# Kernel optimization log

Hardware: AMD Instinct MI355X
Metric: run time of the kernel (lower is better)

## Reference

```python
import jax, jax.numpy as jnp
import numpy as np

B, D, C, H, L = 32768, 64, 64, 1024, 6
EPS = 1e-5
NIN = (D - D // 2) + C  # unchanged half + cond = 96
SPLIT = D // 2          # 32


def setup_inputs() -> dict:
    key = jax.random.key(0)
    ks = jax.random.split(key, 12)
    s = 0.05
    return {
        "z": jax.random.normal(ks[0], (B, D), jnp.float32),
        "cond": jax.random.normal(ks[1], (B, C), jnp.float32),
        "W1": jax.random.normal(ks[2], (L, NIN, H), jnp.float32) * s,
        "b1": jax.random.normal(ks[3], (L, H), jnp.float32) * s,
        "W2": jax.random.normal(ks[4], (L, H, H), jnp.float32) * s,
        "b2": jax.random.normal(ks[5], (L, H), jnp.float32) * s,
        "Ws": jax.random.normal(ks[6], (L, H, SPLIT), jnp.float32) * s,
        "bs": jax.random.normal(ks[7], (L, SPLIT), jnp.float32) * s,
        "Wt": jax.random.normal(ks[8], (L, H, SPLIT), jnp.float32) * s,
        "bt": jax.random.normal(ks[9], (L, SPLIT), jnp.float32) * s,
        "bn_w": 1.0 + 0.1 * jax.random.normal(ks[10], (L, D), jnp.float32),
        "bn_b": 0.1 * jax.random.normal(ks[11], (L, D), jnp.float32),
    }


def reference(z, cond, W1, b1, W2, b2, Ws, bs, Wt, bt, bn_w, bn_b):
    x = z
    log_det = jnp.zeros((z.shape[0],), z.dtype)
    for i in range(L):
        # 'even' mask keeps even indices on even layers, odd indices otherwise
        if i % 2 == 0:
            keep, chg = np.arange(0, D, 2), np.arange(1, D, 2)
        else:
            keep, chg = np.arange(1, D, 2), np.arange(0, D, 2)
        # 2-layer MLP on [x_keep, cond]
        h = jax.nn.relu(jnp.concatenate([x[:, keep], cond], axis=1) @ W1[i] + b1[i])
        h = jax.nn.relu(h @ W2[i] + b2[i])
        log_s = jnp.tanh(h @ Ws[i] + bs[i])          # (B, SPLIT)
        t = h @ Wt[i] + bt[i]                         # (B, SPLIT)
        x2t = x[:, chg] * jnp.exp(log_s) + t
        x = jnp.zeros_like(x).at[:, keep].set(x[:, keep]).at[:, chg].set(x2t)
        log_det = log_det + log_s.sum(axis=1)
        # BatchNorm1d, training mode: batch mean / biased variance, eps=1e-5
        mean = x.mean(axis=0)
        var = x.var(axis=0)
        x = (x - mean) * jax.lax.rsqrt(var + EPS) * bn_w[i] + bn_b[i]
        log_det = log_det + jnp.log(jnp.abs(bn_w[i])).sum()
    return x, log_det
```

## Files before the change

kernel.cpp:

```cpp
#include <hip/hip_runtime.h>
#include <math.h>

#define BB 32768
#define DD 64
#define CC 64
#define HH 1024
#define LL 6
#define SPLIT 32
#define NIN 96
#define EPSV 1e-5f

typedef short short8 __attribute__((ext_vector_type(8)));
typedef float f32x4 __attribute__((ext_vector_type(4)));
typedef unsigned short u16;

__device__ __forceinline__ u16 f2bf(float f) {
    union { float f; unsigned int u; } c; c.f = f;
    unsigned int u = c.u + 0x7FFFu + ((c.u >> 16) & 1u);
    return (u16)(u >> 16);
}

__device__ __forceinline__ void gl_lds16(const u16* g, u16* l) {
    __builtin_amdgcn_global_load_lds(
        (const __attribute__((address_space(1))) unsigned int*)g,
        (__attribute__((address_space(3))) unsigned int*)l, 16, 0, 0);
}

#define DSR(dst, addr, off) \
    asm volatile("ds_read_b128 %0, %1 offset:" #off : "=&v"(dst) : "v"(addr))

__global__ void transpose_cvt_kernel(const float* __restrict__ src, u16* __restrict__ dst,
                                     int R, int C, int Rpad,
                                     long long sstride, long long dstride)
{
    __shared__ float tile[32][33];
    const float* s = src + (size_t)blockIdx.z * sstride;
    u16* d = dst + (size_t)blockIdx.z * dstride;
    int r0 = blockIdx.x * 32, c0 = blockIdx.y * 32;
    int tc = threadIdx.x & 31, tr = threadIdx.x >> 5;
#pragma unroll
    for (int i = 0; i < 4; ++i) {
        int r = r0 + tr + i * 8;
        tile[tr + i * 8][tc] = (r < R) ? s[(size_t)r * C + c0 + tc] : 0.f;
    }
    __syncthreads();
#pragma unroll
    for (int i = 0; i < 4; ++i) {
        int cc = tr + i * 8;
        d[(size_t)(c0 + cc) * Rpad + r0 + tc] = f2bf(tile[tc][cc]);
    }
}

__global__ __launch_bounds__(256)
void init_ain_cond_kernel(const float* __restrict__ cond, u16* __restrict__ Ain)
{
    int t = blockIdx.x * 256 + threadIdx.x;
    int c = t % 96, r = t / 96;
    Ain[(size_t)r * 128 + 32 + c] = (c < CC) ? f2bf(cond[(size_t)r * CC + c]) : (u16)0;
}

__global__ __launch_bounds__(256)
void build_keep_kernel(const float* __restrict__ x, u16* __restrict__ Ain, int keep_off)
{
    int t = blockIdx.x * 256 + threadIdx.x;
    int c = t & 31, r = t >> 5;
    Ain[(size_t)r * 128 + c] = f2bf(x[(size_t)r * DD + 2 * c + keep_off]);
}

__global__ __launch_bounds__(512, 2)
void gemm_tiled(const u16* __restrict__ A,
                const u16* __restrict__ Bt,
                const float* __restrict__ bias,
                u16* __restrict__ Cc,
                int K)
{
    __shared__ u16 sA[2][32 * 512];
    __shared__ u16 sB[2][32 * 512];

    const int t = threadIdx.x;
    const int w = t >> 6, lane = t & 63;
    const int lane16 = lane & 15, quad = lane >> 4;
    const int wm = w >> 2, wn = w & 3;

    int id = blockIdx.x;
    int nby = gridDim.x >> 2;
    int xcd = id & 7, slot = id >> 3;
    int bx = slot & 3, byq = slot >> 2;
    int by = xcd * (nby >> 3) + byq;
    const int bm = by * 256, bn = bx * 256;

    const int ntile = K >> 6;

    auto stage_half = [&](int kt, int op, int s, int buf) {
        int k0 = kt * 64 + s * 32 + quad * 8;
#pragma unroll
        for (int r = 0; r < 2; ++r) {
            int i = r * 8 + w;
            int e = s * 16 + i;
            if (op == 0) {
                const u16* g = A + (size_t)(bm + i * 16 + lane16) * K + k0;
                gl_lds16(g, &sA[buf][e * 512]);
            } else {
                const u16* g = Bt + (size_t)(bn + i * 16 + lane16) * K + k0;
                gl_lds16(g, &sB[buf][e * 512]);
            }
        }
    };

    f32x4 acc[8][4];
#pragma unroll
    for (int a = 0; a < 8; ++a)
#pragma unroll
        for (int b = 0; b < 4; ++b) acc[a][b] = (f32x4){0.f, 0.f, 0.f, 0.f};

    const unsigned sAb = (unsigned)(size_t)(__attribute__((address_space(3))) u16*)&sA[0][0];
    const unsigned sBb = (unsigned)(size_t)(__attribute__((address_space(3))) u16*)&sB[0][0];
    const unsigned aoff = (unsigned)(wm * 8 * 1024 + lane * 16);
    const unsigned boff = (unsigned)(wn * 4 * 1024 + lane * 16);

    stage_half(0, 0, 0, 0);
    stage_half(0, 1, 0, 0);
    stage_half(0, 0, 1, 0);
    stage_half(0, 1, 1, 0);
    asm volatile("s_waitcnt vmcnt(4)");
    __builtin_amdgcn_s_barrier();

    short8 af[4], ag[4], bf[4], bg[4];
    for (int kt = 0; kt < ntile; ++kt) {
        const unsigned base = (unsigned)((kt & 1) << 15);
        const unsigned aA0 = sAb + base + aoff;
        const unsigned aB0 = sBb + base + boff;
        const unsigned aA1 = aA0 + 16384;
        const unsigned aB1 = aB0 + 16384;
        const int nk = (kt + 1 < ntile) ? kt + 1 : kt;
        const int nb = (kt + 1) & 1;

        DSR(bf[0], aB0, 0); DSR(bf[1], aB0, 1024);
        DSR(bf[2], aB0, 2048); DSR(bf[3], aB0, 3072);
        DSR(af[0], aA0, 0); DSR(af[1], aA0, 1024);
        DSR(af[2], aA0, 2048); DSR(af[3], aA0, 3072);
        stage_half(nk, 0, 0, nb);
        __builtin_amdgcn_s_barrier();
        asm volatile("s_waitcnt lgkmcnt(0)");
        __builtin_amdgcn_sched_barrier(0);
        __builtin_amdgcn_s_setprio(1);
#pragma unroll
        for (int a = 0; a < 4; ++a)
#pragma unroll
            for (int b = 0; b < 4; ++b)
                acc[a][b] = __builtin_amdgcn_mfma_f32_16x16x32_bf16(af[a], bf[b], acc[a][b], 0, 0, 0);
        __builtin_amdgcn_s_setprio(0);
        __builtin_amdgcn_s_barrier();

        DSR(ag[0], aA0, 4096); DSR(ag[1], aA0, 5120);
        DSR(ag[2], aA0, 6144); DSR(ag[3], aA0, 7168);
        stage_half(nk, 1, 0, nb);
        __builtin_amdgcn_s_barrier();
        asm volatile("s_waitcnt lgkmcnt(0)");
        __builtin_amdgcn_sched_barrier(0);
        __builtin_amdgcn_s_setprio(1);
#pragma unroll
        for (int a = 0; a < 4; ++a)
#pragma unroll
            for (int b = 0; b < 4; ++b)
                acc[4 + a][b] = __builtin_amdgcn_mfma_f32_16x16x32_bf16(ag[a], bf[b], acc[4 + a][b], 0, 0, 0);
        __builtin_amdgcn_s_setprio(0);
        asm volatile("s_waitcnt vmcnt(4)");
        __builtin_amdgcn_s_barrier();

        DSR(bg[0], aB1, 0); DSR(bg[1], aB1, 1024);
        DSR(bg[2], aB1, 2048); DSR(bg[3], aB1, 3072);
        DSR(af[0], aA1, 0); DSR(af[1], aA1, 1024);
        DSR(af[2], aA1, 2048); DSR(af[3], aA1, 3072);
        stage_half(nk, 0, 1, nb);
        __builtin_amdgcn_s_barrier();
        asm volatile("s_waitcnt lgkmcnt(0)");
        __builtin_amdgcn_sched_barrier(0);
        __builtin_amdgcn_s_setprio(1);
#pragma unroll
        for (int a = 0; a < 4; ++a)
#pragma unroll
            for (int b = 0; b < 4; ++b)
                acc[a][b] = __builtin_amdgcn_mfma_f32_16x16x32_bf16(af[a], bg[b], acc[a][b], 0, 0, 0);
        __builtin_amdgcn_s_setprio(0);
        __builtin_amdgcn_s_barrier();

        DSR(ag[0], aA1, 4096); DSR(ag[1], aA1, 5120);
        DSR(ag[2], aA1, 6144); DSR(ag[3], aA1, 7168);
        stage_half(nk, 1, 1, nb);
        __builtin_amdgcn_s_barrier();
        asm volatile("s_waitcnt lgkmcnt(0)");
        __builtin_amdgcn_sched_barrier(0);
        __builtin_amdgcn_s_setprio(1);
#pragma unroll
        for (int a = 0; a < 4; ++a)
#pragma unroll
            for (int b = 0; b < 4; ++b)
                acc[4 + a][b] = __builtin_amdgcn_mfma_f32_16x16x32_bf16(ag[a], bg[b], acc[4 + a][b], 0, 0, 0);
        __builtin_amdgcn_s_setprio(0);
        asm volatile("s_waitcnt vmcnt(4)");
        __builtin_amdgcn_s_barrier();
    }
    __syncthreads();

    constexpr int ES = 72;
    float bv[4];
#pragma unroll
    for (int b = 0; b < 4; ++b) bv[b] = bias[bn + wn * 64 + b * 16 + lane16];
    u16* scr = ((u16*)sB) + w * (16 * ES);
#pragma unroll
    for (int a = 0; a < 8; ++a) {
#pragma unroll
        for (int b = 0; b < 4; ++b)
#pragma unroll
            for (int r = 0; r < 4; ++r) {
                float v = fmaxf(acc[a][b][r] + bv[b], 0.f);
                scr[(quad * 4 + r) * ES + b * 16 + lane16] = f2bf(v);
            }
#pragma unroll
        for (int ch = 0; ch < 2; ++ch) {
            int row = ch * 8 + (lane >> 3), colc = (lane & 7) * 8;
            short8 v = *(const short8*)(scr + row * ES + colc);
            *(short8*)(Cc + (size_t)(bm + wm * 128 + a * 16 + row) * 1024 + bn + wn * 64 + colc) = v;
        }
    }
}

__global__ __launch_bounds__(512)
void gemm3_coupling(const u16* __restrict__ A,
                    const u16* __restrict__ Bt,
                    const float* __restrict__ bs, const float* __restrict__ bt,
                    float* __restrict__ x, float* __restrict__ log_det,
                    float* __restrict__ stat_sum, float* __restrict__ stat_sumsq,
                    int keep_off, int row0)
{
    constexpr int ST_STRIDE = 66;
    __shared__ u16 stg[2][24 * 512];
    __shared__ float ssum[8][64], ssum2[8][64];
    float* sst = (float*)stg;

    const int t = threadIdx.x;
    const int w = t >> 6, lane = t & 63;
    const int lane16 = lane & 15, quad = lane >> 4;
    const int wm = w >> 1, wn = w & 1;
    const int bm = blockIdx.x * 128;

    auto stage = [&](int it, int buf) {
        int k0 = it * 64;
#pragma unroll
        for (int p = 0; p < 3; ++p) {
            int e = w + p * 8;
            if (e < 16) {
                int s = e >> 3, i = e & 7;
                const u16* g = A + (size_t)(bm + i * 16 + lane16) * HH + (k0 + s * 32 + quad * 8);
                gl_lds16(g, &stg[buf][e * 512]);
            } else {
                int j2 = e - 16, s = j2 >> 2, j = j2 & 3;
                const u16* g = Bt + (size_t)(j * 16 + lane16) * HH + (k0 + s * 32 + quad * 8);
                gl_lds16(g, &stg[buf][e * 512]);
            }
        }
    };

    f32x4 acc[2][2];
#pragma unroll
    for (int a = 0; a < 2; ++a)
#pragma unroll
        for (int b = 0; b < 2; ++b) acc[a][b] = (f32x4){0.f, 0.f, 0.f, 0.f};

    stage(0, 0);
    for (int it = 0; it < 16; ++it) {
        const int buf = it & 1;
        __syncthreads();
        if (it + 1 < 16) stage(it + 1, buf ^ 1);
        u16* ldsA = stg[buf];
        u16* ldsB = stg[buf] + 16 * 512;
#pragma unroll
        for (int s = 0; s < 2; ++s) {
            short8 af[2], bfr[2];
#pragma unroll
            for (int a = 0; a < 2; ++a)
                af[a] = *(const short8*)(ldsA + ((s * 8 + wm * 2 + a) * 512) + lane * 8);
#pragma unroll
            for (int b = 0; b < 2; ++b)
                bfr[b] = *(const short8*)(ldsB + ((s * 4 + wn * 2 + b) * 512) + lane * 8);
#pragma unroll
            for (int a = 0; a < 2; ++a)
#pragma unroll
                for (int b = 0; b < 2; ++b)
                    acc[a][b] = __builtin_amdgcn_mfma_f32_16x16x32_bf16(af[a], bfr[b], acc[a][b], 0, 0, 0);
        }
    }
    __syncthreads();

#pragma unroll
    for (int a = 0; a < 2; ++a)
#pragma unroll
        for (int b = 0; b < 2; ++b)
#pragma unroll
            for (int r = 0; r < 4; ++r) {
                int row = wm * 32 + a * 16 + quad * 4 + r;
                int col = wn * 32 + b * 16 + lane16;
                sst[row * ST_STRIDE + col] = acc[a][b][r];
            }
    __syncthreads();

    const int f = lane;
    const bool is_chg = ((f & 1) != keep_off);
    const int j = f >> 1;
    float bsj = 0.f, btj = 0.f;
    if (is_chg) { bsj = bs[j]; btj = bt[j]; }

    float lsum = 0.f, lsum2 = 0.f;
    for (int i = 0; i < 16; ++i) {
        int crow = w * 16 + i;
        int grow = row0 + bm + crow;
        float xv = x[(size_t)grow * DD + f];
        float ld = 0.f;
        if (is_chg) {
            float s_raw = sst[crow * ST_STRIDE + j];
            float t_raw = sst[crow * ST_STRIDE + SPLIT + j];
            float ls = tanhf(s_raw + bsj);
            float tv = t_raw + btj;
            xv = xv * expf(ls) + tv;
            x[(size_t)grow * DD + f] = xv;
            ld = ls;
        }
        for (int off = 32; off > 0; off >>= 1) ld += __shfl_down(ld, off, 64);
        if (f == 0) log_det[grow] += ld;
        lsum  += xv;
        lsum2 += xv * xv;
    }

    ssum[w][f]  = lsum;
    ssum2[w][f] = lsum2;
    __syncthreads();
    if (t < 64) {
        float a = 0.f, b = 0.f;
#pragma unroll
        for (int g = 0; g < 8; ++g) { a += ssum[g][t]; b += ssum2[g][t]; }
        atomicAdd(stat_sum + t, a);
        atomicAdd(stat_sumsq + t, b);
    }
}

__global__ __launch_bounds__(256)
void normalize_kernel(const float* __restrict__ xin, float* __restrict__ xout,
                      const float* __restrict__ stat_sum, const float* __restrict__ stat_sumsq,
                      const float* __restrict__ bn_w, const float* __restrict__ bn_b,
                      float* __restrict__ log_det,
                      u16* __restrict__ Ain, int off_next)
{
    __shared__ float sscale[64], sshift[64], scsum;
    int t = threadIdx.x;
    if (t < 64) {
        const float invB = 1.f / (float)BB;
        float mean = stat_sum[t] * invB;
        float var  = stat_sumsq[t] * invB - mean * mean;
        float inv  = rsqrtf(var + EPSV);
        float wv   = bn_w[t];
        float sc   = inv * wv;
        sscale[t] = sc;
        sshift[t] = bn_b[t] - mean * sc;
        float lg = logf(fabsf(wv));
        for (int off = 32; off > 0; off >>= 1) lg += __shfl_down(lg, off, 64);
        if (t == 0) scsum = lg;
    }
    __syncthreads();

    int idx = blockIdx.x * blockDim.x + t;
    int f0 = (idx & 15) * 4;
    int row = idx >> 4;
    float4 v = ((const float4*)xin)[idx];
    v.x = v.x * sscale[f0 + 0] + sshift[f0 + 0];
    v.y = v.y * sscale[f0 + 1] + sshift[f0 + 1];
    v.z = v.z * sscale[f0 + 2] + sshift[f0 + 2];
    v.w = v.w * sscale[f0 + 3] + sshift[f0 + 3];
    ((float4*)xout)[idx] = v;
    if ((idx & 15) == 0) log_det[row] += scsum;
    if (Ain) {
        float a0 = off_next ? v.y : v.x;
        float a1 = off_next ? v.w : v.z;
        ushort2 u; u.x = f2bf(a0); u.y = f2bf(a1);
        *(ushort2*)(Ain + (size_t)row * 128 + (f0 >> 1)) = u;
    }
}

extern "C" void kernel_launch(void* const* d_in, const int* in_sizes, int n_in,
                              void* d_out, int out_size, void* d_ws, size_t ws_size,
                              hipStream_t stream)
{
    const float* z    = (const float*)d_in[0];
    const float* cond = (const float*)d_in[1];
    const float* W1   = (const float*)d_in[2];
    const float* b1   = (const float*)d_in[3];
    const float* W2   = (const float*)d_in[4];
    const float* b2   = (const float*)d_in[5];
    const float* Ws   = (const float*)d_in[6];
    const float* bs   = (const float*)d_in[7];
    const float* Wt   = (const float*)d_in[8];
    const float* bt   = (const float*)d_in[9];
    const float* bn_w = (const float*)d_in[10];
    const float* bn_b = (const float*)d_in[11];

    float* out_x  = (float*)d_out;
    float* out_ld = out_x + (size_t)BB * DD;

    char* p = (char*)d_ws;
    size_t used = 0;
    auto alloc = [&](size_t bytes) { void* q = p + used; used += (bytes + 255) & ~(size_t)255; return q; };

    float* xbuf = (float*)alloc((size_t)BB * DD * 4);
    u16*   w1t  = (u16*)alloc((size_t)LL * HH * 128 * 2);
    u16*   w2t  = (u16*)alloc((size_t)LL * HH * HH * 2);
    u16*   wstt = (u16*)alloc((size_t)LL * 64 * HH * 2);
    u16*   Ain  = (u16*)alloc((size_t)BB * 128 * 2);
    float* stat_sum   = (float*)alloc(64 * 4);
    float* stat_sumsq = (float*)alloc(64 * 4);

    int CH = BB;
    while (CH > 8192 && used + (size_t)CH * 4096 + 4096 > ws_size) CH >>= 1;
    u16* h1 = (u16*)alloc((size_t)CH * HH * 2);
    u16* h2 = (u16*)alloc((size_t)CH * HH * 2);

    hipMemcpyAsync(xbuf, z, (size_t)BB * DD * sizeof(float), hipMemcpyDeviceToDevice, stream);
    hipMemsetAsync(out_ld, 0, (size_t)BB * sizeof(float), stream);

    transpose_cvt_kernel<<<dim3(128/32, HH/32, LL), 256, 0, stream>>>(
        W1, w1t, NIN, HH, 128, (long long)NIN * HH, (long long)HH * 128);
    transpose_cvt_kernel<<<dim3(HH/32, HH/32, LL), 256, 0, stream>>>(
        W2, w2t, HH, HH, HH, (long long)HH * HH, (long long)HH * HH);
    transpose_cvt_kernel<<<dim3(HH/32, SPLIT/32, LL), 256, 0, stream>>>(
        Ws, wstt, HH, SPLIT, HH, (long long)HH * SPLIT, (long long)64 * HH);
    transpose_cvt_kernel<<<dim3(HH/32, SPLIT/32, LL), 256, 0, stream>>>(
        Wt, wstt + (size_t)SPLIT * HH, HH, SPLIT, HH, (long long)HH * SPLIT, (long long)64 * HH);

    init_ain_cond_kernel<<<BB * 96 / 256, 256, 0, stream>>>(cond, Ain);
    build_keep_kernel<<<BB * 32 / 256, 256, 0, stream>>>(xbuf, Ain, 0);

    for (int l = 0; l < LL; ++l) {
        const int off = l & 1;
        hipMemsetAsync(stat_sum, 0, 2 * 64 * sizeof(float), stream);

        for (int c = 0; c < BB / CH; ++c) {
            const int row0 = c * CH;

            gemm_tiled<<<(CH / 256) * 4, 512, 0, stream>>>(
                Ain + (size_t)row0 * 128, w1t + (size_t)l * HH * 128,
                b1 + (size_t)l * HH, h1, 128);

            gemm_tiled<<<(CH / 256) * 4, 512, 0, stream>>>(
                h1, w2t + (size_t)l * HH * HH,
                b2 + (size_t)l * HH, h2, HH);

            gemm3_coupling<<<CH / 128, 512, 0, stream>>>(
                h2, wstt + (size_t)l * 64 * HH,
                bs + (size_t)l * SPLIT, bt + (size_t)l * SPLIT,
                xbuf, out_ld, stat_sum, stat_sumsq, off, row0);
        }

        float* xout = (l == LL - 1) ? out_x : xbuf;
        u16* ain_next = (l < LL - 1) ? Ain : nullptr;
        normalize_kernel<<<(BB * DD / 4) / 256, 256, 0, stream>>>(
            xbuf, xout, stat_sum, stat_sumsq,
            bn_w + (size_t)l * DD, bn_b + (size_t)l * DD,
            out_ld, ain_next, (l + 1) & 1);
    }
}
```

Measured before the change: 961.2 us.

## Preload full Ws/Wt weight tile into LDS and stream A rows from global

The third GEMM (hidden to scale/shift) in the coupling kernel now loads the entire 64x1024 bf16 B operand into LDS once, instead of double-buffering A and B tiles across 16 synchronised iterations. Each wave owns 16 rows and reads its A fragments directly from global memory, with no LDS staging or per-iteration barriers. The intent is to remove the staging barriers and LDS traffic for A. In exchange the kernel uses 128 KB of LDS, which limits occupancy to about one block per CU, and global A loads are exposed without explicit prefetch.

```diff
diff --git a/kernel.cpp b/kernel.cpp
--- a/kernel.cpp
+++ b/kernel.cpp
@@ -235,74 +235,48 @@
                     int keep_off, int row0)
 {
     constexpr int ST_STRIDE = 66;
-    __shared__ u16 stg[2][24 * 512];
+    __shared__ u16 sB[128 * 512];
     __shared__ float ssum[8][64], ssum2[8][64];
-    float* sst = (float*)stg;
+    float* sst = (float*)sB;
 
     const int t = threadIdx.x;
     const int w = t >> 6, lane = t & 63;
     const int lane16 = lane & 15, quad = lane >> 4;
-    const int wm = w >> 1, wn = w & 1;
     const int bm = blockIdx.x * 128;
 
-    auto stage = [&](int it, int buf) {
-        int k0 = it * 64;
-#pragma unroll
-        for (int p = 0; p < 3; ++p) {
-            int e = w + p * 8;
-            if (e < 16) {
-                int s = e >> 3, i = e & 7;
-                const u16* g = A + (size_t)(bm + i * 16 + lane16) * HH + (k0 + s * 32 + quad * 8);
-                gl_lds16(g, &stg[buf][e * 512]);
-            } else {
-                int j2 = e - 16, s = j2 >> 2, j = j2 & 3;
-                const u16* g = Bt + (size_t)(j * 16 + lane16) * HH + (k0 + s * 32 + quad * 8);
-                gl_lds16(g, &stg[buf][e * 512]);
-            }
+#pragma unroll
+    for (int r = 0; r < 16; ++r) {
+        int e = r * 8 + w;
+        int s = e >> 2, j = e & 3;
+        const u16* g = Bt + (size_t)(j * 16 + lane16) * HH + s * 32 + quad * 8;
+        gl_lds16(g, &sB[e * 512]);
+    }
+
+    f32x4 acc[4];
+#pragma unroll
+    for (int j = 0; j < 4; ++j) acc[j] = (f32x4){0.f, 0.f, 0.f, 0.f};
+
+    const u16* Arow = A + (size_t)(bm + w * 16 + lane16) * HH + quad * 8;
+
+    __syncthreads();
+
+#pragma unroll 4
+    for (int s = 0; s < 32; ++s) {
+        short8 af = *(const short8*)(Arow + s * 32);
+        const u16* bb = sB + s * 2048 + lane * 8;
+#pragma unroll
+        for (int j = 0; j < 4; ++j) {
+            short8 bfr = *(const short8*)(bb + j * 512);
+            acc[j] = __builtin_amdgcn_mfma_f32_16x16x32_bf16(af, bfr, acc[j], 0, 0, 0);
         }
-    };
-
-    f32x4 acc[2][2];
-#pragma unroll
-    for (int a = 0; a < 2; ++a)
-#pragma unroll
-        for (int b = 0; b < 2; ++b) acc[a][b] = (f32x4){0.f, 0.f, 0.f, 0.f};
-
-    stage(0, 0);
-    for (int it = 0; it < 16; ++it) {
-        const int buf = it & 1;
-        __syncthreads();
-        if (it + 1 < 16) stage(it + 1, buf ^ 1);
-        u16* ldsA = stg[buf];
-        u16* ldsB = stg[buf] + 16 * 512;
-#pragma unroll
-        for (int s = 0; s < 2; ++s) {
-            short8 af[2], bfr[2];
-#pragma unroll
-            for (int a = 0; a < 2; ++a)
-                af[a] = *(const short8*)(ldsA + ((s * 8 + wm * 2 + a) * 512) + lane * 8);
-#pragma unroll
-            for (int b = 0; b < 2; ++b)
-                bfr[b] = *(const short8*)(ldsB + ((s * 4 + wn * 2 + b) * 512) + lane * 8);
-#pragma unroll
-            for (int a = 0; a < 2; ++a)
-#pragma unroll
-                for (int b = 0; b < 2; ++b)
-                    acc[a][b] = __builtin_amdgcn_mfma_f32_16x16x32_bf16(af[a], bfr[b], acc[a][b], 0, 0, 0);
-        }
-    }
-    __syncthreads();
-
-#pragma unroll
-    for (int a = 0; a < 2; ++a)
-#pragma unroll
-        for (int b = 0; b < 2; ++b)
-#pragma unroll
-            for (int r = 0; r < 4; ++r) {
-                int row = wm * 32 + a * 16 + quad * 4 + r;
-                int col = wn * 32 + b * 16 + lane16;
-                sst[row * ST_STRIDE + col] = acc[a][b][r];
-            }
+    }
+    __syncthreads();
+
+#pragma unroll
+    for (int j = 0; j < 4; ++j)
+#pragma unroll
+        for (int r = 0; r < 4; ++r)
+            sst[(w * 16 + quad * 4 + r) * ST_STRIDE + j * 16 + lane16] = acc[j][r];
     __syncthreads();
 
     const int f = lane;
```

New measurement: 945.0 us. No clear change (-1.7%).
